# Kernel optimization log

Hardware: AMD Instinct MI355X
Metric: run time of the kernel (lower is better)

Reference implementation:

```python
import jax, jax.numpy as jnp
import numpy as np

B, S, N, IN_D = 16, 12, 2048, 2
H, HEADS, DH = 64, 4, 16
E = 32768
DT = 0.1            # encoder_scale * seq_in / (encoder_interval*seq_in) steps
STEPS = 12          # encoder_interval * seq_in
NEG_SLOPE = 0.2


def setup_inputs() -> dict:
    key = jax.random.key(0)
    ks = jax.random.split(key, 12)
    s = 1.0 / np.sqrt(H)
    return {
        "inputs": jax.random.normal(ks[0], (B, S, N, IN_D), jnp.float32),
        "w_in": jax.random.normal(ks[1], (IN_D, H), jnp.float32) / np.sqrt(IN_D),
        "b_in": jnp.zeros((H,), jnp.float32),
        "Wh": jax.random.normal(ks[2], (H, H), jnp.float32) * s,
        "bias_g": jnp.zeros((H,), jnp.float32),
        "a_src": jax.random.normal(ks[3], (HEADS, DH), jnp.float32) * s,
        "a_dst": jax.random.normal(ks[4], (HEADS, DH), jnp.float32) * s,
        "w1": jax.random.normal(ks[5], (H, H), jnp.float32) * s,
        "b1": jnp.zeros((H,), jnp.float32),
        "w2": jax.random.normal(ks[6], (H, H), jnp.float32) * s,
        "b2": jnp.zeros((H,), jnp.float32),
        "src": jax.random.randint(ks[7], (E,), 0, N, jnp.int32),
        "dst": jax.random.randint(ks[8], (E,), 0, N, jnp.int32),
    }


def _gat(y, Wh, bias_g, a_src, a_dst, src, dst):
    """Single-layer multi-head GAT: dy/dt. y: [B,N,H]."""
    h = (y @ Wh).reshape(B, N, HEADS, DH)                      # [B,N,h,d]
    e_s = jnp.einsum('bnhd,hd->bnh', h, a_src)                 # [B,N,h]
    e_d = jnp.einsum('bnhd,hd->bnh', h, a_dst)
    # per-edge attention logits, leading edge axis for segment ops
    e = jax.nn.leaky_relu(e_s[:, src] + e_d[:, dst], NEG_SLOPE)  # [B,E,h]
    e = jnp.transpose(e, (1, 0, 2))                            # [E,B,h]
    m = jax.ops.segment_max(e, dst, num_segments=N)            # [N,B,h]
    w = jnp.exp(e - m[dst])
    denom = jax.ops.segment_sum(w, dst, num_segments=N)        # [N,B,h]
    alpha = w / denom[dst]                                     # [E,B,h]
    h_src = jnp.transpose(h[:, src], (1, 0, 2, 3))             # [E,B,h,d]
    agg = jax.ops.segment_sum(alpha[..., None] * h_src, dst, num_segments=N)  # [N,B,h,d]
    out = jnp.transpose(agg, (1, 0, 2, 3)).reshape(B, N, H) + bias_g
    return out


def reference(inputs, w_in, b_in, Wh, bias_g, a_src, a_dst, w1, b1, w2, b2, src, dst):
    x = inputs @ w_in + b_in            # [B,S,N,H]
    y0 = x[:, 0]                        # [B,N,H]  (initial state at t=0)

    f = lambda y: _gat(y, Wh, bias_g, a_src, a_dst, src, dst)

    def rk4_step(y, _):
        k1 = f(y)
        k2 = f(y + 0.5 * DT * k1)
        k3 = f(y + 0.5 * DT * k2)
        k4 = f(y + DT * k3)
        y = y + (DT / 6.0) * (k1 + 2.0 * k2 + 2.0 * k3 + k4)
        return y, None

    y, _ = jax.lax.scan(rk4_step, y0, None, length=STEPS)
    out = jnp.tanh(y @ w1 + b1) @ w2 + b2   # output_layer: Linear-Tanh-Linear
    return out
```

## Files before the change

### kernel.cpp

```cpp
#include <hip/hip_runtime.h>

#define NB 16
#define NS 12
#define NN 2048
#define NE 32768
#define NROWS (NB*NN)
#define DTC  0.1f
#define DT2C 0.05f
#define DT6C (0.1f/6.0f)
#define LOG2E 1.44269504088896f


__device__ __forceinline__ unsigned short f2bf(float f) {
    unsigned int u = __float_as_uint(f);
    u = u + 0x7fffu + ((u >> 16) & 1u);
    return (unsigned short)(u >> 16);
}
__device__ __forceinline__ float fexp2(float x) {
#if __has_builtin(__builtin_amdgcn_exp2f)
    return __builtin_amdgcn_exp2f(x);
#else
    return __expf(x * 0.69314718056f);
#endif
}

__global__ __launch_bounds__(256) void init_y_k(const float* __restrict__ inputs,
    const float* __restrict__ w_in, const float* __restrict__ b_in, float* __restrict__ y)
{
    int idx = blockIdx.x * 256 + threadIdx.x;
    int hh = idx & 63;
    int tn = idx >> 6;
    int n = tn >> 4, b = tn & 15;
    const float* ip = inputs + ((size_t)(b * NS) * NN + n) * 2;
    y[idx] = ip[0] * w_in[hh] + ip[1] * w_in[64 + hh] + b_in[hh];
}

__global__ __launch_bounds__(256) void zero_deg_k(int* __restrict__ deg)
{
    int i = blockIdx.x * 256 + threadIdx.x;
    if (i < NN) deg[i] = 0;
}
__global__ __launch_bounds__(256) void count_deg_k(const int* __restrict__ dst, int* __restrict__ deg)
{
    int e = blockIdx.x * 256 + threadIdx.x;
    if (e < NE) atomicAdd(&deg[dst[e]], 1);
}
__global__ __launch_bounds__(1024) void scan_k(const int* __restrict__ deg,
    int* __restrict__ offs, int* __restrict__ cursor)
{
    __shared__ int p[1024];
    int t = threadIdx.x;
    int d0 = deg[2 * t], d1 = deg[2 * t + 1];
    p[t] = d0 + d1;
    __syncthreads();
    for (int d = 1; d < 1024; d <<= 1) {
        int v = (t >= d) ? p[t - d] : 0;
        __syncthreads();
        p[t] += v;
        __syncthreads();
    }
    int excl = (t > 0) ? p[t - 1] : 0;
    offs[2 * t] = excl;       offs[2 * t + 1] = excl + d0;
    cursor[2 * t] = excl;     cursor[2 * t + 1] = excl + d0;
    if (t == 1023) offs[2048] = p[1023];
}
__global__ __launch_bounds__(256) void scatter_k(const int* __restrict__ src, const int* __restrict__ dst,
    int* __restrict__ cursor, int* __restrict__ csr)
{
    int e = blockIdx.x * 256 + threadIdx.x;
    if (e < NE) {
        int pos = atomicAdd(&cursor[dst[e]], 1);
        csr[pos] = src[e];
    }
}

__global__ __launch_bounds__(1024, 8) void fused_k(
    const float* yin, float* __restrict__ acc, float* yout,
    const uint2* __restrict__ htR, const float* __restrict__ estR, const float* __restrict__ edtR,
    uint2* __restrict__ htW, float* __restrict__ estW, float* __restrict__ edtW,
    const int* __restrict__ offs, const int* __restrict__ csr, const float* __restrict__ bias_g,
    const float* __restrict__ Wh, const float* __restrict__ a_src, const float* __restrict__ a_dst,
    int mode)
{
    __shared__ float kvs[64 * 64];
    __shared__ float Zs[64 * 65];
    __shared__ unsigned int Hs[64 * 33];
    __shared__ float Ps[16][64];
    __shared__ float Pd[16][64];

    int t = threadIdx.x;
    int lane = t & 63;
    int wid = __builtin_amdgcn_readfirstlane(t >> 6);

    if (mode != 0) {
        int np = wid >> 2, bg = wid & 3;
        int n = blockIdx.x * 4 + np;
        int hd = lane >> 4;
        int o0 = offs[n], o1 = offs[n + 1];
        int eoff = bg * 16 + (lane & 15);
        float edv = edtR[(size_t)n * 64 + eoff];
        const uint2* hbase = htR + (size_t)bg * 64 + lane;

        float d0 = 0.f, d1 = 0.f, d2 = 0.f, d3 = 0.f;
        float a0 = 0.f, a1 = 0.f, a2 = 0.f, a3 = 0.f;
        for (int base = o0; base < o1; base += 64) {
            int cnt = o1 - base; if (cnt > 64) cnt = 64;
            int svv = csr[base + (lane < cnt ? lane : cnt - 1)];
#pragma unroll 2
            for (int j = 0; j < cnt; j++) {
                int s = __builtin_amdgcn_readlane(svv, j);
                float esv = estR[(size_t)s * 64 + eoff];
                float e = esv + edv;
                e = fmaxf(e, 0.2f * e);
                float w = fexp2(e);
                float w0 = __shfl(w, hd);
                float w1 = __shfl(w, 4 + hd);
                float w2 = __shfl(w, 8 + hd);
                float w3 = __shfl(w, 12 + hd);
                uint2 hv = hbase[(size_t)s * 256];
                float h0 = __uint_as_float(hv.x << 16);
                float h1 = __uint_as_float(hv.x & 0xffff0000u);
                float h2 = __uint_as_float(hv.y << 16);
                float h3 = __uint_as_float(hv.y & 0xffff0000u);
                d0 += w0; a0 += w0 * h0;
                d1 += w1; a1 += w1 * h1;
                d2 += w2; a2 += w2 * h2;
                d3 += w3; a3 += w3 * h3;
            }
        }
        float bgb = bias_g[lane];
        bool has = (o1 > o0);
        float r0 = has ? __builtin_amdgcn_rcpf(d0) : 0.f;
        float r1 = has ? __builtin_amdgcn_rcpf(d1) : 0.f;
        float r2 = has ? __builtin_amdgcn_rcpf(d2) : 0.f;
        float r3 = has ? __builtin_amdgcn_rcpf(d3) : 0.f;
        int rb = np * 16 + bg * 4;
        kvs[(rb + 0) * 64 + lane] = a0 * r0 + bgb;
        kvs[(rb + 1) * 64 + lane] = a1 * r1 + bgb;
        kvs[(rb + 2) * 64 + lane] = a2 * r2 + bgb;
        kvs[(rb + 3) * 64 + lane] = a3 * r3 + bgb;
        __syncthreads();
    }

    int row0 = blockIdx.x * 64;
    const float4* y4 = (const float4*)(yin + (size_t)row0 * 64);
    float4* a4g = (float4*)(acc + (size_t)row0 * 64);
    float4* yo4 = (float4*)(yout + (size_t)row0 * 64);
    int flat = t;
    float4 z = y4[flat];
    if (mode >= 1) {
        float4 kf = *(const float4*)&kvs[flat * 4];
        if (mode == 1) {
            a4g[flat] = kf;
            z.x += DT2C * kf.x; z.y += DT2C * kf.y; z.z += DT2C * kf.z; z.w += DT2C * kf.w;
        } else if (mode == 2) {
            float4 av = a4g[flat];
            av.x += 2.f * kf.x; av.y += 2.f * kf.y; av.z += 2.f * kf.z; av.w += 2.f * kf.w;
            a4g[flat] = av;
            z.x += DT2C * kf.x; z.y += DT2C * kf.y; z.z += DT2C * kf.z; z.w += DT2C * kf.w;
        } else if (mode == 3) {
            float4 av = a4g[flat];
            av.x += 2.f * kf.x; av.y += 2.f * kf.y; av.z += 2.f * kf.z; av.w += 2.f * kf.w;
            a4g[flat] = av;
            z.x += DTC * kf.x; z.y += DTC * kf.y; z.z += DTC * kf.z; z.w += DTC * kf.w;
        } else {
            float4 av = a4g[flat];
            z.x += DT6C * (av.x + kf.x); z.y += DT6C * (av.y + kf.y);
            z.z += DT6C * (av.z + kf.z); z.w += DT6C * (av.w + kf.w);
            yo4[flat] = z;
        }
    }
    if (mode == 5) return;

    {
        int r = flat >> 4;
        int kkb = (flat & 15) << 2;
        Zs[(kkb + 0) * 65 + r] = z.x;
        Zs[(kkb + 1) * 65 + r] = z.y;
        Zs[(kkb + 2) * 65 + r] = z.z;
        Zs[(kkb + 3) * 65 + r] = z.w;
    }
    __syncthreads();

    const float* wcol = Wh + wid * 4;
    float a0 = 0.f, a1 = 0.f, a2 = 0.f, a3 = 0.f;
    for (int kk = 0; kk < 64; kk++) {
        float zk = Zs[kk * 65 + lane];
        const float4* w4 = (const float4*)(wcol + kk * 64);
        float4 w = w4[0];
        a0 += zk * w.x; a1 += zk * w.y; a2 += zk * w.z; a3 += zk * w.w;
    }

    Hs[lane * 33 + wid * 2 + 0] = (unsigned int)f2bf(a0) | ((unsigned int)f2bf(a1) << 16);
    Hs[lane * 33 + wid * 2 + 1] = (unsigned int)f2bf(a2) | ((unsigned int)f2bf(a3) << 16);

    int head = wid >> 2, qp = wid & 3;
    const float* as = a_src + head * 16 + qp * 4;
    const float* ad = a_dst + head * 16 + qp * 4;
    Ps[wid][lane] = a0 * as[0] + a1 * as[1] + a2 * as[2] + a3 * as[3];
    Pd[wid][lane] = a0 * ad[0] + a1 * ad[1] + a2 * ad[2] + a3 * ad[3];
    __syncthreads();

    if (wid < 4) {
        int tn = row0 + lane;
        float sv = (Ps[wid * 4 + 0][lane] + Ps[wid * 4 + 1][lane]
                  + Ps[wid * 4 + 2][lane] + Ps[wid * 4 + 3][lane]) * LOG2E;
        float dv = (Pd[wid * 4 + 0][lane] + Pd[wid * 4 + 1][lane]
                  + Pd[wid * 4 + 2][lane] + Pd[wid * 4 + 3][lane]) * LOG2E;
        estW[(size_t)tn * 4 + wid] = sv;
        edtW[(size_t)tn * 4 + wid] = dv;
    }

    if (t < 512) {
        int nbg = t >> 5;
        int np = nbg >> 2, bg = nbg & 3;
        int cp = t & 31;
        int rbase = np * 16 + bg * 4;
        unsigned int r0 = Hs[(rbase + 0) * 33 + cp];
        unsigned int r1 = Hs[(rbase + 1) * 33 + cp];
        unsigned int r2 = Hs[(rbase + 2) * 33 + cp];
        unsigned int r3 = Hs[(rbase + 3) * 33 + cp];
        uint4 o;
        o.x = (r0 & 0xffffu) | (r1 << 16);
        o.y = (r2 & 0xffffu) | (r3 << 16);
        o.z = (r0 >> 16) | (r1 & 0xffff0000u);
        o.w = (r2 >> 16) | (r3 & 0xffff0000u);
        int ng = blockIdx.x * 4 + np;
        *(uint4*)((unsigned int*)htW + (((size_t)(ng * 4 + bg)) * 64 + 2 * cp) * 2) = o;
    }
}

__global__ __launch_bounds__(256) void mlp_k(
    const float* __restrict__ yin,
    const float* __restrict__ w1, const float* __restrict__ b1,
    const float* __restrict__ w2, const float* __restrict__ b2,
    float* __restrict__ out)
{
    __shared__ float Zs[64 * 65];
    __shared__ float Ts[64 * 65];
    int t = threadIdx.x;
    int row0 = blockIdx.x * 64;
    const float4* y4 = (const float4*)(yin + (size_t)row0 * 64);
#pragma unroll
    for (int i = 0; i < 4; i++) {
        int flat = t + 256 * i;
        float4 z = y4[flat];
        int r = flat >> 4;
        int kkb = (flat & 15) << 2;
        Zs[(kkb + 0) * 65 + r] = z.x;
        Zs[(kkb + 1) * 65 + r] = z.y;
        Zs[(kkb + 2) * 65 + r] = z.z;
        Zs[(kkb + 3) * 65 + r] = z.w;
    }
    __syncthreads();

    int lane = t & 63;
    int g = __builtin_amdgcn_readfirstlane(t >> 6);
    float a[16];
#pragma unroll
    for (int j = 0; j < 16; j++) a[j] = 0.f;
    const float* w1g = w1 + g * 16;
    for (int kk = 0; kk < 64; kk++) {
        float zk = Zs[kk * 65 + lane];
        const float4* w4 = (const float4*)(w1g + kk * 64);
        float4 w0 = w4[0], w1v = w4[1], w2v = w4[2], w3v = w4[3];
        a[0] += zk * w0.x;  a[1] += zk * w0.y;  a[2] += zk * w0.z;  a[3] += zk * w0.w;
        a[4] += zk * w1v.x; a[5] += zk * w1v.y; a[6] += zk * w1v.z; a[7] += zk * w1v.w;
        a[8] += zk * w2v.x; a[9] += zk * w2v.y; a[10] += zk * w2v.z; a[11] += zk * w2v.w;
        a[12] += zk * w3v.x; a[13] += zk * w3v.y; a[14] += zk * w3v.z; a[15] += zk * w3v.w;
    }
    const float4* b1g = (const float4*)(b1 + g * 16);
    float4 bb0 = b1g[0], bb1 = b1g[1], bb2 = b1g[2], bb3 = b1g[3];
    float bb[16] = { bb0.x,bb0.y,bb0.z,bb0.w, bb1.x,bb1.y,bb1.z,bb1.w,
                     bb2.x,bb2.y,bb2.z,bb2.w, bb3.x,bb3.y,bb3.z,bb3.w };
#pragma unroll
    for (int j = 0; j < 16; j++) {
        float v = a[j] + bb[j];
        float ex = __expf(2.f * v);
        float tv = 1.f - 2.f / (ex + 1.f);
        Ts[(16 * g + j) * 65 + lane] = tv;
    }
    __syncthreads();

    float a2[16];
#pragma unroll
    for (int j = 0; j < 16; j++) a2[j] = 0.f;
    const float* w2g = w2 + g * 16;
    for (int kk = 0; kk < 64; kk++) {
        float tk = Ts[kk * 65 + lane];
        const float4* w4 = (const float4*)(w2g + kk * 64);
        float4 w0 = w4[0], w1v = w4[1], w2v = w4[2], w3v = w4[3];
        a2[0] += tk * w0.x;  a2[1] += tk * w0.y;  a2[2] += tk * w0.z;  a2[3] += tk * w0.w;
        a2[4] += tk * w1v.x; a2[5] += tk * w1v.y; a2[6] += tk * w1v.z; a2[7] += tk * w1v.w;
        a2[8] += tk * w2v.x; a2[9] += tk * w2v.y; a2[10] += tk * w2v.z; a2[11] += tk * w2v.w;
        a2[12] += tk * w3v.x; a2[13] += tk * w3v.y; a2[14] += tk * w3v.z; a2[15] += tk * w3v.w;
    }
    const float4* b2g = (const float4*)(b2 + g * 16);
    float4 c0 = b2g[0], c1 = b2g[1], c2 = b2g[2], c3 = b2g[3];
    int tn = row0 + lane;
    int n = tn >> 4, b = tn & 15;
    float4* o4 = (float4*)(out + ((size_t)b * NN + n) * 64 + g * 16);
    o4[0] = make_float4(a2[0] + c0.x, a2[1] + c0.y, a2[2] + c0.z, a2[3] + c0.w);
    o4[1] = make_float4(a2[4] + c1.x, a2[5] + c1.y, a2[6] + c1.z, a2[7] + c1.w);
    o4[2] = make_float4(a2[8] + c2.x, a2[9] + c2.y, a2[10] + c2.z, a2[11] + c2.w);
    o4[3] = make_float4(a2[12] + c3.x, a2[13] + c3.y, a2[14] + c3.z, a2[15] + c3.w);
}

extern "C" void kernel_launch(void* const* d_in, const int* in_sizes, int n_in,
                              void* d_out, int out_size, void* d_ws, size_t ws_size,
                              hipStream_t stream)
{
    const float* inputs = (const float*)d_in[0];
    const float* w_in   = (const float*)d_in[1];
    const float* b_in   = (const float*)d_in[2];
    const float* Wh     = (const float*)d_in[3];
    const float* bias_g = (const float*)d_in[4];
    const float* a_src  = (const float*)d_in[5];
    const float* a_dst  = (const float*)d_in[6];
    const float* w1     = (const float*)d_in[7];
    const float* b1     = (const float*)d_in[8];
    const float* w2     = (const float*)d_in[9];
    const float* b2     = (const float*)d_in[10];
    const int* src      = (const int*)d_in[11];
    const int* dst      = (const int*)d_in[12];
    float* out = (float*)d_out;

    float* ws = (float*)d_ws;
    const size_t SZ = (size_t)NROWS * 64;
    float* y   = ws;
    float* acc = y + SZ;
    uint2* htA = (uint2*)(acc + SZ);
    float* estA = (float*)((unsigned short*)htA + SZ);
    float* edtA = estA + (size_t)NROWS * 4;
    uint2* htB = (uint2*)(edtA + (size_t)NROWS * 4);
    float* estB = (float*)((unsigned short*)htB + SZ);
    float* edtB = estB + (size_t)NROWS * 4;
    int* offs   = (int*)(edtB + (size_t)NROWS * 4);
    int* cursor = offs + 2064;
    int* deg    = cursor + 2048;
    int* csr    = deg + 2048;

    init_y_k<<<NROWS * 64 / 256, 256, 0, stream>>>(inputs, w_in, b_in, y);
    zero_deg_k<<<8, 256, 0, stream>>>(deg);
    count_deg_k<<<NE / 256, 256, 0, stream>>>(dst, deg);
    scan_k<<<1, 1024, 0, stream>>>(deg, offs, cursor);
    scatter_k<<<NE / 256, 256, 0, stream>>>(src, dst, cursor, csr);

    uint2* htR = htA;  float* estR = estA; float* edtR = edtA;
    uint2* htW = htB;  float* estW = estB; float* edtW = edtB;

    fused_k<<<512, 1024, 0, stream>>>(y, acc, y, htB, estB, edtB, htA, estA, edtA,
                                      offs, csr, bias_g, Wh, a_src, a_dst, 0);
    for (int step = 0; step < 12; step++) {
        for (int st = 1; st <= 4; st++) {
            int mode = (step == 11 && st == 4) ? 5 : st;
            fused_k<<<512, 1024, 0, stream>>>(y, acc, y, htR, estR, edtR, htW, estW, edtW,
                                              offs, csr, bias_g, Wh, a_src, a_dst, mode);
            uint2* th = htR; htR = htW; htW = th;
            float* te = estR; estR = estW; estW = te;
            float* td = edtR; edtR = edtW; edtW = td;
        }
    }
    mlp_k<<<512, 256, 0, stream>>>(y, w1, b1, w2, b2, out);
}
```

Baseline: 1.054 ms.

## Pad CSR segments to multiples of eight and batch edge gathers

Each node's degree is rounded up to a multiple of eight, and the padding slots point to a dummy node N whose source logits are set to -1e30, so padded edges get zero weight. This lets the edge loop process eight neighbors per iteration with no bounds check. All eight logit and feature gathers are issued before any of the math, which raises memory-level parallelism and hides gather latency. The cost is extra buffer space for the dummy row and some wasted work on padded edges.

New measurement: 1.071 ms. About the same (+1.6%).

```diff
diff --git a/kernel.cpp b/kernel.cpp
--- a/kernel.cpp
+++ b/kernel.cpp
@@ -9,6 +9,7 @@
 #define DT2C 0.05f
 #define DT6C (0.1f/6.0f)
 #define LOG2E 1.44269504088896f
+#define CSRCAP 49152
 
 
 __device__ __forceinline__ unsigned short f2bf(float f) {
@@ -35,10 +36,16 @@
     y[idx] = ip[0] * w_in[hh] + ip[1] * w_in[64 + hh] + b_in[hh];
 }
 
-__global__ __launch_bounds__(256) void zero_deg_k(int* __restrict__ deg)
-{
-    int i = blockIdx.x * 256 + threadIdx.x;
-    if (i < NN) deg[i] = 0;
+__global__ __launch_bounds__(256) void prep_k(int* __restrict__ deg, int* __restrict__ csr,
+    float* __restrict__ estA, float* __restrict__ estB)
+{
+    int t = blockIdx.x * 256 + threadIdx.x;
+    if (t < NN) deg[t] = 0;
+    if (t < CSRCAP) csr[t] = NN;
+    if (t < 64) {
+        estA[(size_t)NN * 64 + t] = -1e30f;
+        estB[(size_t)NN * 64 + t] = -1e30f;
+    }
 }
 __global__ __launch_bounds__(256) void count_deg_k(const int* __restrict__ dst, int* __restrict__ deg)
 {
@@ -50,7 +57,8 @@
 {
     __shared__ int p[1024];
     int t = threadIdx.x;
-    int d0 = deg[2 * t], d1 = deg[2 * t + 1];
+    int d0 = (deg[2 * t] + 7) & ~7;
+    int d1 = (deg[2 * t + 1] + 7) & ~7;
     p[t] = d0 + d1;
     __syncthreads();
     for (int d = 1; d < 1024; d <<= 1) {
@@ -106,26 +114,34 @@
         for (int base = o0; base < o1; base += 64) {
             int cnt = o1 - base; if (cnt > 64) cnt = 64;
             int svv = csr[base + (lane < cnt ? lane : cnt - 1)];
-#pragma unroll 2
-            for (int j = 0; j < cnt; j++) {
-                int s = __builtin_amdgcn_readlane(svv, j);
-                float esv = estR[(size_t)s * 64 + eoff];
-                float e = esv + edv;
-                e = fmaxf(e, 0.2f * e);
-                float w = fexp2(e);
-                float w0 = __shfl(w, hd);
-                float w1 = __shfl(w, 4 + hd);
-                float w2 = __shfl(w, 8 + hd);
-                float w3 = __shfl(w, 12 + hd);
-                uint2 hv = hbase[(size_t)s * 256];
-                float h0 = __uint_as_float(hv.x << 16);
-                float h1 = __uint_as_float(hv.x & 0xffff0000u);
-                float h2 = __uint_as_float(hv.y << 16);
-                float h3 = __uint_as_float(hv.y & 0xffff0000u);
-                d0 += w0; a0 += w0 * h0;
-                d1 += w1; a1 += w1 * h1;
-                d2 += w2; a2 += w2 * h2;
-                d3 += w3; a3 += w3 * h3;
+            for (int j = 0; j < cnt; j += 8) {
+                int ss[8];
+                float es8[8];
+                uint2 hv8[8];
+#pragma unroll
+                for (int q = 0; q < 8; q++) ss[q] = __builtin_amdgcn_readlane(svv, j + q);
+#pragma unroll
+                for (int q = 0; q < 8; q++) es8[q] = estR[(size_t)ss[q] * 64 + eoff];
+#pragma unroll
+                for (int q = 0; q < 8; q++) hv8[q] = hbase[(size_t)ss[q] * 256];
+#pragma unroll
+                for (int q = 0; q < 8; q++) {
+                    float e = es8[q] + edv;
+                    e = fmaxf(e, 0.2f * e);
+                    float w = fexp2(e);
+                    float w0 = __shfl(w, hd);
+                    float w1 = __shfl(w, 4 + hd);
+                    float w2 = __shfl(w, 8 + hd);
+                    float w3 = __shfl(w, 12 + hd);
+                    float h0 = __uint_as_float(hv8[q].x << 16);
+                    float h1 = __uint_as_float(hv8[q].x & 0xffff0000u);
+                    float h2 = __uint_as_float(hv8[q].y << 16);
+                    float h3 = __uint_as_float(hv8[q].y & 0xffff0000u);
+                    d0 += w0; a0 += w0 * h0;
+                    d1 += w1; a1 += w1 * h1;
+                    d2 += w2; a2 += w2 * h2;
+                    d3 += w3; a3 += w3 * h3;
+                }
             }
         }
         float bgb = bias_g[lane];
@@ -327,21 +343,24 @@
 
     float* ws = (float*)d_ws;
     const size_t SZ = (size_t)NROWS * 64;
+    const size_t HTU = 525312;
+    const size_t ESF = 131136;
+    const size_t EDF = 131072;
     float* y   = ws;
     float* acc = y + SZ;
     uint2* htA = (uint2*)(acc + SZ);
-    float* estA = (float*)((unsigned short*)htA + SZ);
-    float* edtA = estA + (size_t)NROWS * 4;
-    uint2* htB = (uint2*)(edtA + (size_t)NROWS * 4);
-    float* estB = (float*)((unsigned short*)htB + SZ);
-    float* edtB = estB + (size_t)NROWS * 4;
-    int* offs   = (int*)(edtB + (size_t)NROWS * 4);
+    float* estA = (float*)(htA + HTU);
+    float* edtA = estA + ESF;
+    uint2* htB = (uint2*)(edtA + EDF);
+    float* estB = (float*)(htB + HTU);
+    float* edtB = estB + ESF;
+    int* offs   = (int*)(edtB + EDF);
     int* cursor = offs + 2064;
     int* deg    = cursor + 2048;
     int* csr    = deg + 2048;
 
     init_y_k<<<NROWS * 64 / 256, 256, 0, stream>>>(inputs, w_in, b_in, y);
-    zero_deg_k<<<8, 256, 0, stream>>>(deg);
+    prep_k<<<CSRCAP / 256, 256, 0, stream>>>(deg, csr, estA, estB);
     count_deg_k<<<NE / 256, 256, 0, stream>>>(dst, deg);
     scan_k<<<1, 1024, 0, stream>>>(deg, offs, cursor);
     scatter_k<<<NE / 256, 256, 0, stream>>>(src, dst, cursor, csr);
```
